# Kernel optimization log

Hardware: AMD Instinct MI355X
Metric: run time of the kernel (lower is better)

Reference implementation:

```python
import jax, jax.numpy as jnp
import numpy as np

# Irreps: in1 = in2 = out = 8x0e + 8x1o  (mul_ir / e3nn layout: [scalars(8) | vectors(8,3)])
MUL = 8
DIM = 4 * MUL           # 8*1 + 8*3 = 32
NPATH = 4               # (0e,0e->0e), (1o,1o->0e), (0e,1o->1o), (1o,0e->1o)
WNUM = NPATH * MUL**3   # 2048
BATCH = 1 << 20

# Real O3 Clebsch-Gordan values (component normalization, e3nn convention):
#   C(0e,0e->0e) = 1 ;  C(1o,1o->0e)_ij = delta_ij / sqrt(3)
#   C(0e,1o->1o)_jk = delta_jk ;  C(1o,0e->1o)_ik = delta_ik
INV_SQRT3 = 1.0 / np.sqrt(3.0)
# Path normalization: each output irrep receives 2 paths with fan-in mul*mul each
ALPHA = 1.0 / np.sqrt(2.0 * MUL * MUL)


def setup_inputs() -> dict:
    key = jax.random.key(0)
    k1, k2, k3 = jax.random.split(key, 3)
    x1 = jax.random.normal(k1, (BATCH, DIM), dtype=jnp.float32)
    x2 = jax.random.normal(k2, (BATCH, DIM), dtype=jnp.float32)
    weight = jax.random.normal(k3, (1, WNUM), dtype=jnp.float32)
    return {"x1": x1, "x2": x2, "weight": weight}


def reference(x1, x2, weight):
    B = x1.shape[0]
    n = MUL ** 3
    w = weight[0]
    # per-path fully-connected weights, each (mul1, mul2, mul3)
    W0 = w[0 * n:1 * n].reshape(MUL, MUL, MUL)  # 0e x 0e -> 0e
    W1 = w[1 * n:2 * n].reshape(MUL, MUL, MUL)  # 1o x 1o -> 0e
    W2 = w[2 * n:3 * n].reshape(MUL, MUL, MUL)  # 0e x 1o -> 1o
    W3 = w[3 * n:4 * n].reshape(MUL, MUL, MUL)  # 1o x 0e -> 1o

    s1 = x1[:, :MUL]                       # (B, 8) scalars
    v1 = x1[:, MUL:].reshape(B, MUL, 3)    # (B, 8, 3) vectors
    s2 = x2[:, :MUL]
    v2 = x2[:, MUL:].reshape(B, MUL, 3)

    # 0e output: scalar*scalar path + vector-dot path (CG = delta_ij/sqrt(3))
    out0 = (jnp.einsum('bu,bv,uvw->bw', s1, s2, W0)
            + INV_SQRT3 * jnp.einsum('bui,bvi,uvw->bw', v1, v2, W1))
    # 1o output: scalar*vector paths (CG = identity on the vector index)
    out1 = (jnp.einsum('bu,bvk,uvw->bwk', s1, v2, W2)
            + jnp.einsum('buk,bv,uvw->bwk', v1, s2, W3))

    out = jnp.concatenate([out0, out1.reshape(B, 3 * MUL)], axis=-1)
    return ALPHA * out
```

## Files before the change

kernel.cpp:

```cpp
#include <hip/hip_runtime.h>


constexpr int TPB = 256;

__global__ __launch_bounds__(TPB) void tp_kernel(
    const float* __restrict__ x1,
    const float* __restrict__ x2,
    const float* __restrict__ wg,
    float* __restrict__ out,
    int batch)
{
    const float INV3  = 0.57735026918962576f;
    const float ALPHA = 0.088388347648318447f;

    __shared__ alignas(16) float W[2048];

    int b = blockIdx.x * TPB + threadIdx.x;

    float X1[32], X2[32];
    {
        const float4* p1 = (const float4*)(x1 + (size_t)b * 32);
        const float4* p2 = (const float4*)(x2 + (size_t)b * 32);
        #pragma unroll
        for (int j = 0; j < 8; ++j) {
            float4 t1 = p1[j];
            X1[4*j+0] = t1.x; X1[4*j+1] = t1.y; X1[4*j+2] = t1.z; X1[4*j+3] = t1.w;
            float4 t2 = p2[j];
            X2[4*j+0] = t2.x; X2[4*j+1] = t2.y; X2[4*j+2] = t2.z; X2[4*j+3] = t2.w;
        }
    }

    {
        const float4* ws = (const float4*)wg;
        float4* wd = (float4*)W;
        int t = threadIdx.x;
        wd[t]       = ws[t];
        wd[t + 256] = ws[t + 256];
    }
    __syncthreads();

    if (b >= batch) return;

    float acc0[8], acc0b[8], acc1[8][3];
    #pragma unroll
    for (int t = 0; t < 8; ++t) {
        acc0[t] = 0.f; acc0b[t] = 0.f;
        acc1[t][0] = 0.f; acc1[t][1] = 0.f; acc1[t][2] = 0.f;
    }

    #pragma unroll
    for (int v = 0; v < 8; ++v) {
        float s2v = X2[v];
        float c0 = X2[8+v*3+0], c1 = X2[8+v*3+1], c2 = X2[8+v*3+2];
        float e[8];
        #pragma unroll
        for (int t = 0; t < 8; ++t) e[t] = 0.f;

        #pragma unroll
        for (int u = 0; u < 8; ++u) {
            float s1u = X1[u];
            float p = s1u * s2v;
            float d = X1[8+u*3+0]*c0 + X1[8+u*3+1]*c1 + X1[8+u*3+2]*c2;
            const float4* w0 = (const float4*)&W[u*64 + v*8];
            const float4* w1 = (const float4*)&W[512 + u*64 + v*8];
            const float4* w2 = (const float4*)&W[1024 + u*64 + v*8];
            float4 a0 = w0[0], b0 = w0[1];
            float4 a1 = w1[0], b1 = w1[1];
            float4 a2 = w2[0], b2 = w2[1];
            acc0[0] += p*a0.x; acc0[1] += p*a0.y; acc0[2] += p*a0.z; acc0[3] += p*a0.w;
            acc0[4] += p*b0.x; acc0[5] += p*b0.y; acc0[6] += p*b0.z; acc0[7] += p*b0.w;
            acc0b[0] += d*a1.x; acc0b[1] += d*a1.y; acc0b[2] += d*a1.z; acc0b[3] += d*a1.w;
            acc0b[4] += d*b1.x; acc0b[5] += d*b1.y; acc0b[6] += d*b1.z; acc0b[7] += d*b1.w;
            e[0] += s1u*a2.x; e[1] += s1u*a2.y; e[2] += s1u*a2.z; e[3] += s1u*a2.w;
            e[4] += s1u*b2.x; e[5] += s1u*b2.y; e[6] += s1u*b2.z; e[7] += s1u*b2.w;
        }
        #pragma unroll
        for (int t = 0; t < 8; ++t) {
            acc1[t][0] += c0 * e[t];
            acc1[t][1] += c1 * e[t];
            acc1[t][2] += c2 * e[t];
        }
    }

    #pragma unroll
    for (int u = 0; u < 8; ++u) {
        float f[8];
        #pragma unroll
        for (int t = 0; t < 8; ++t) f[t] = 0.f;
        #pragma unroll
        for (int v = 0; v < 8; ++v) {
            float sv = X2[v];
            const float4* w3 = (const float4*)&W[1536 + u*64 + v*8];
            float4 a3 = w3[0], b3 = w3[1];
            f[0] += sv*a3.x; f[1] += sv*a3.y; f[2] += sv*a3.z; f[3] += sv*a3.w;
            f[4] += sv*b3.x; f[5] += sv*b3.y; f[6] += sv*b3.z; f[7] += sv*b3.w;
        }
        float c0 = X1[8+u*3+0], c1 = X1[8+u*3+1], c2 = X1[8+u*3+2];
        #pragma unroll
        for (int t = 0; t < 8; ++t) {
            acc1[t][0] += c0 * f[t];
            acc1[t][1] += c1 * f[t];
            acc1[t][2] += c2 * f[t];
        }
    }

    float O[32];
    #pragma unroll
    for (int t = 0; t < 8; ++t) O[t] = ALPHA * (acc0[t] + INV3 * acc0b[t]);
    #pragma unroll
    for (int t = 0; t < 8; ++t) {
        O[8 + t*3 + 0] = ALPHA * acc1[t][0];
        O[8 + t*3 + 1] = ALPHA * acc1[t][1];
        O[8 + t*3 + 2] = ALPHA * acc1[t][2];
    }
    float4* po = (float4*)(out + (size_t)b * 32);
    #pragma unroll
    for (int j = 0; j < 8; ++j) {
        po[j] = make_float4(O[4*j+0], O[4*j+1], O[4*j+2], O[4*j+3]);
    }
}

extern "C" void kernel_launch(void* const* d_in, const int* in_sizes, int n_in,
                              void* d_out, int out_size, void* d_ws, size_t ws_size,
                              hipStream_t stream) {
    const float* x1 = (const float*)d_in[0];
    const float* x2 = (const float*)d_in[1];
    const float* wg = (const float*)d_in[2];
    float* out = (float*)d_out;

    int batch = in_sizes[0] / 32;
    dim3 grid((batch + TPB - 1) / TPB), block(TPB);
    hipLaunchKernelGGL(tp_kernel, grid, block, 0, stream, x1, x2, wg, out, batch);
}
```

Baseline: 444.9 us.

## Read weights directly from global as uniform loads and use packed FMA

```diff
diff --git a/kernel.cpp b/kernel.cpp
--- a/kernel.cpp
+++ b/kernel.cpp
@@ -1,5 +1,7 @@
 #include <hip/hip_runtime.h>
 
+
+typedef float v2f __attribute__((ext_vector_type(2)));
 
 constexpr int TPB = 256;
 
@@ -13,9 +15,8 @@
     const float INV3  = 0.57735026918962576f;
     const float ALPHA = 0.088388347648318447f;
 
-    __shared__ alignas(16) float W[2048];
-
     int b = blockIdx.x * TPB + threadIdx.x;
+    if (b >= batch) return;
 
     float X1[32], X2[32];
     {
@@ -30,88 +31,85 @@
         }
     }
 
-    {
-        const float4* ws = (const float4*)wg;
-        float4* wd = (float4*)W;
-        int t = threadIdx.x;
-        wd[t]       = ws[t];
-        wd[t + 256] = ws[t + 256];
-    }
-    __syncthreads();
-
-    if (b >= batch) return;
-
-    float acc0[8], acc0b[8], acc1[8][3];
+    v2f acc0[4], acc0b[4], a01[8];
+    float a2[8];
     #pragma unroll
-    for (int t = 0; t < 8; ++t) {
-        acc0[t] = 0.f; acc0b[t] = 0.f;
-        acc1[t][0] = 0.f; acc1[t][1] = 0.f; acc1[t][2] = 0.f;
-    }
+    for (int j = 0; j < 4; ++j) { acc0[j] = (v2f){0.f,0.f}; acc0b[j] = (v2f){0.f,0.f}; }
+    #pragma unroll
+    for (int t = 0; t < 8; ++t) { a01[t] = (v2f){0.f,0.f}; a2[t] = 0.f; }
 
     #pragma unroll
     for (int v = 0; v < 8; ++v) {
         float s2v = X2[v];
         float c0 = X2[8+v*3+0], c1 = X2[8+v*3+1], c2 = X2[8+v*3+2];
-        float e[8];
-        #pragma unroll
-        for (int t = 0; t < 8; ++t) e[t] = 0.f;
+        v2f cc01 = {c0, c1};
+        v2f e[4] = {{0.f,0.f},{0.f,0.f},{0.f,0.f},{0.f,0.f}};
 
         #pragma unroll
         for (int u = 0; u < 8; ++u) {
             float s1u = X1[u];
             float p = s1u * s2v;
             float d = X1[8+u*3+0]*c0 + X1[8+u*3+1]*c1 + X1[8+u*3+2]*c2;
-            const float4* w0 = (const float4*)&W[u*64 + v*8];
-            const float4* w1 = (const float4*)&W[512 + u*64 + v*8];
-            const float4* w2 = (const float4*)&W[1024 + u*64 + v*8];
-            float4 a0 = w0[0], b0 = w0[1];
-            float4 a1 = w1[0], b1 = w1[1];
-            float4 a2 = w2[0], b2 = w2[1];
-            acc0[0] += p*a0.x; acc0[1] += p*a0.y; acc0[2] += p*a0.z; acc0[3] += p*a0.w;
-            acc0[4] += p*b0.x; acc0[5] += p*b0.y; acc0[6] += p*b0.z; acc0[7] += p*b0.w;
-            acc0b[0] += d*a1.x; acc0b[1] += d*a1.y; acc0b[2] += d*a1.z; acc0b[3] += d*a1.w;
-            acc0b[4] += d*b1.x; acc0b[5] += d*b1.y; acc0b[6] += d*b1.z; acc0b[7] += d*b1.w;
-            e[0] += s1u*a2.x; e[1] += s1u*a2.y; e[2] += s1u*a2.z; e[3] += s1u*a2.w;
-            e[4] += s1u*b2.x; e[5] += s1u*b2.y; e[6] += s1u*b2.z; e[7] += s1u*b2.w;
+            v2f pp = {p, p}, dd = {d, d}, ss = {s1u, s1u};
+            const v2f* w0 = (const v2f*)(wg +         u*64 + v*8);
+            const v2f* w1 = (const v2f*)(wg +  512 +  u*64 + v*8);
+            const v2f* w2 = (const v2f*)(wg + 1024 +  u*64 + v*8);
+            #pragma unroll
+            for (int j = 0; j < 4; ++j) {
+                acc0[j]  = __builtin_elementwise_fma(pp, w0[j], acc0[j]);
+                acc0b[j] = __builtin_elementwise_fma(dd, w1[j], acc0b[j]);
+                e[j]     = __builtin_elementwise_fma(ss, w2[j], e[j]);
+            }
         }
         #pragma unroll
-        for (int t = 0; t < 8; ++t) {
-            acc1[t][0] += c0 * e[t];
-            acc1[t][1] += c1 * e[t];
-            acc1[t][2] += c2 * e[t];
+        for (int j = 0; j < 4; ++j) {
+            float e0 = e[j].x, e1 = e[j].y;
+            v2f ee0 = {e0, e0}, ee1 = {e1, e1};
+            a01[2*j]   = __builtin_elementwise_fma(cc01, ee0, a01[2*j]);
+            a01[2*j+1] = __builtin_elementwise_fma(cc01, ee1, a01[2*j+1]);
+            a2[2*j]   += c2 * e0;
+            a2[2*j+1] += c2 * e1;
         }
     }
 
     #pragma unroll
     for (int u = 0; u < 8; ++u) {
-        float f[8];
-        #pragma unroll
-        for (int t = 0; t < 8; ++t) f[t] = 0.f;
+        v2f f[4] = {{0.f,0.f},{0.f,0.f},{0.f,0.f},{0.f,0.f}};
         #pragma unroll
         for (int v = 0; v < 8; ++v) {
             float sv = X2[v];
-            const float4* w3 = (const float4*)&W[1536 + u*64 + v*8];
-            float4 a3 = w3[0], b3 = w3[1];
-            f[0] += sv*a3.x; f[1] += sv*a3.y; f[2] += sv*a3.z; f[3] += sv*a3.w;
-            f[4] += sv*b3.x; f[5] += sv*b3.y; f[6] += sv*b3.z; f[7] += sv*b3.w;
+            v2f ss = {sv, sv};
+            const v2f* w3 = (const v2f*)(wg + 1536 + u*64 + v*8);
+            #pragma unroll
+            for (int j = 0; j < 4; ++j)
+                f[j] = __builtin_elementwise_fma(ss, w3[j], f[j]);
         }
         float c0 = X1[8+u*3+0], c1 = X1[8+u*3+1], c2 = X1[8+u*3+2];
+        v2f cc01 = {c0, c1};
         #pragma unroll
-        for (int t = 0; t < 8; ++t) {
-            acc1[t][0] += c0 * f[t];
-            acc1[t][1] += c1 * f[t];
-            acc1[t][2] += c2 * f[t];
+        for (int j = 0; j < 4; ++j) {
+            float f0 = f[j].x, f1 = f[j].y;
+            v2f ff0 = {f0, f0}, ff1 = {f1, f1};
+            a01[2*j]   = __builtin_elementwise_fma(cc01, ff0, a01[2*j]);
+            a01[2*j+1] = __builtin_elementwise_fma(cc01, ff1, a01[2*j+1]);
+            a2[2*j]   += c2 * f0;
+            a2[2*j+1] += c2 * f1;
         }
     }
 
     float O[32];
     #pragma unroll
-    for (int t = 0; t < 8; ++t) O[t] = ALPHA * (acc0[t] + INV3 * acc0b[t]);
+    for (int j = 0; j < 4; ++j) {
+        v2f iv = {INV3, INV3}, al = {ALPHA, ALPHA};
+        v2f o = al * (acc0[j] + iv * acc0b[j]);
+        O[2*j]   = o.x;
+        O[2*j+1] = o.y;
+    }
     #pragma unroll
     for (int t = 0; t < 8; ++t) {
-        O[8 + t*3 + 0] = ALPHA * acc1[t][0];
-        O[8 + t*3 + 1] = ALPHA * acc1[t][1];
-        O[8 + t*3 + 2] = ALPHA * acc1[t][2];
+        O[8 + t*3 + 0] = ALPHA * a01[t].x;
+        O[8 + t*3 + 1] = ALPHA * a01[t].y;
+        O[8 + t*3 + 2] = ALPHA * a2[t];
     }
     float4* po = (float4*)(out + (size_t)b * 32);
     #pragma unroll
```

New measurement: 369.5 us. 1.2x faster.
